# Kernel tuning notes

Hardware: AMD Instinct MI355X
Metric: run time of the kernel (lower is better)

The kernel has to match this reference:

```python
import jax, jax.numpy as jnp
from jax import lax
import numpy as np

C_IN, C_OUT, K, STRIDE, PAD = 64, 64, 3, 1, 1
EPS = 1e-5


def setup_inputs() -> dict:
    key = jax.random.key(0)
    ks = jax.random.split(key, 6)
    B, H, W = 4, 128, 128
    x = jax.random.normal(ks[0], (B, C_IN, H, W), jnp.float32)
    # small offset weights -> realistic sub-pixel offsets
    offset_w = jax.random.normal(ks[1], (2 * K * K, C_IN, K, K), jnp.float32) * 0.01
    offset_b = jax.random.normal(ks[2], (2 * K * K,), jnp.float32) * 0.01
    dcn_w = jax.random.normal(ks[3], (C_OUT, C_IN, K, K), jnp.float32) / np.sqrt(C_IN * K * K)
    gamma = jax.random.uniform(ks[4], (C_OUT,), jnp.float32, 0.5, 1.5)
    beta = jax.random.normal(ks[5], (C_OUT,), jnp.float32) * 0.1
    return dict(x=x, offset_w=offset_w, offset_b=offset_b, dcn_w=dcn_w, gamma=gamma, beta=beta)


def _bilinear_sample(xb, py, px):
    # xb: (C,H,W); py,px: (K2,Ho,Wo) absolute sample coords (may be out of bounds)
    H, W = xb.shape[1], xb.shape[2]
    y0 = jnp.floor(py); x0 = jnp.floor(px)
    wy = py - y0  # frac weights
    wx = px - x0

    def gather(yi, xi):
        yc = jnp.clip(yi, 0, H - 1).astype(jnp.int32)
        xc = jnp.clip(xi, 0, W - 1).astype(jnp.int32)
        v = xb[:, yc, xc]  # (C,K2,Ho,Wo)
        valid = ((yi >= 0) & (yi <= H - 1) & (xi >= 0) & (xi <= W - 1)).astype(xb.dtype)
        return v * valid[None]

    return (gather(y0, x0) * ((1 - wy) * (1 - wx))[None]
            + gather(y0, x0 + 1) * ((1 - wy) * wx)[None]
            + gather(y0 + 1, x0) * (wy * (1 - wx))[None]
            + gather(y0 + 1, x0 + 1) * (wy * wx)[None])  # (C,K2,Ho,Wo)


def reference(x, offset_w, offset_b, dcn_w, gamma, beta):
    B, C, H, W = x.shape
    K2 = K * K
    # offset conv (standard conv, NCHW)
    offset = lax.conv_general_dilated(
        x, offset_w, (STRIDE, STRIDE), [(PAD, PAD), (PAD, PAD)],
        dimension_numbers=("NCHW", "OIHW", "NCHW")) + offset_b[None, :, None, None]
    Ho, Wo = offset.shape[2], offset.shape[3]
    off = offset.reshape(B, K2, 2, Ho, Wo)  # interleaved (dy, dx) per tap
    dy, dx = off[:, :, 0], off[:, :, 1]
    # base sampling grid: out_pos*stride - pad + kernel tap index
    hs = (jnp.arange(Ho) * STRIDE - PAD).astype(x.dtype)
    ws = (jnp.arange(Wo) * STRIDE - PAD).astype(x.dtype)
    ki, kj = jnp.meshgrid(jnp.arange(K), jnp.arange(K), indexing="ij")
    ki = ki.reshape(K2).astype(x.dtype)
    kj = kj.reshape(K2).astype(x.dtype)
    py = dy + hs[None, None, :, None] + ki[None, :, None, None]  # (B,K2,Ho,Wo)
    px = dx + ws[None, None, None, :] + kj[None, :, None, None]

    sampled = jax.vmap(_bilinear_sample)(x, py, px)  # (B,C,K2,Ho,Wo)
    out = jnp.einsum("bckhw,ock->bohw", sampled, dcn_w.reshape(dcn_w.shape[0], C, K2))

    # BatchNorm (training-mode batch stats) + ReLU
    mean = out.mean((0, 2, 3))
    var = out.var((0, 2, 3))
    out = (out - mean[None, :, None, None]) * lax.rsqrt(var + EPS)[None, :, None, None]
    out = out * gamma[None, :, None, None] + beta[None, :, None, None]
    return jnp.maximum(out, 0.0)
```

## Files before the change

### kernel.cpp

```cpp
#include <hip/hip_runtime.h>

#define HW   16384
#define NPX  65536

typedef unsigned short u16;
typedef unsigned int   u32;
typedef short bf16x8 __attribute__((ext_vector_type(8)));
typedef float f32x4  __attribute__((ext_vector_type(4)));

__device__ __forceinline__ u16 f2b(float f) {
    u32 u = __float_as_uint(f);
    return (u16)((u + 0x7FFFu + ((u >> 16) & 1u)) >> 16);
}
__device__ __forceinline__ float blo(u32 u) { return __uint_as_float(u << 16); }
__device__ __forceinline__ float bhi(u32 u) { return __uint_as_float(u & 0xffff0000u); }

__device__ __forceinline__ u32 comb(u32 a00, u32 a01, u32 a10, u32 a11,
                                    float w00, float w01, float w10, float w11) {
    float lo = fmaf(w11, blo(a11), fmaf(w10, blo(a10), fmaf(w01, blo(a01), w00 * blo(a00))));
    float hi = fmaf(w11, bhi(a11), fmaf(w10, bhi(a10), fmaf(w01, bhi(a01), w00 * bhi(a00))));
    return __builtin_amdgcn_perm(__float_as_uint(hi) + 0x8000u,
                                 __float_as_uint(lo) + 0x8000u, 0x07060302u);
}

#define MFMA __builtin_amdgcn_mfma_f32_16x16x32_bf16
#define NTL(p) __builtin_nontemporal_load(p)

__global__ __launch_bounds__(256)
void k_pre(const float* __restrict__ x, const float* __restrict__ dw,
           const float* __restrict__ ow, u16* __restrict__ xh,
           u16* __restrict__ wtd, u16* __restrict__ wto,
           float* __restrict__ sums) {
    int tid = threadIdx.x;
    int bid = blockIdx.x;
    if (bid >= 512) {
        if (bid == 539) {
            for (int i = tid; i < 1024; i += 256) sums[i] = 0.f;
            return;
        }
        int gid = (bid - 512) * 256 + tid;
        if (gid >= 108 * 64) return;
        int fid = gid >> 6, lane = gid & 63;
        int mi = lane & 15, quad = lane >> 4;
        u32 w[4];
        if (fid < 72) {
            int tap = fid >> 3, rem = fid & 7;
            int ks = rem >> 2, nt = rem & 3;
            int n = nt * 16 + mi;
            int cb = ks * 32 + quad * 8;
#pragma unroll
            for (int i = 0; i < 4; ++i) {
                u32 lo = f2b(dw[(n * 64 + cb + 2 * i) * 9 + tap]);
                u32 hi = f2b(dw[(n * 64 + cb + 2 * i + 1) * 9 + tap]);
                w[i] = lo | (hi << 16);
            }
            *((int4*)wtd + (fid << 6) + lane) = make_int4(w[0], w[1], w[2], w[3]);
        } else {
            int f2 = fid - 72;
            int tap = f2 >> 2, rem = f2 & 3;
            int ks = rem >> 1, nt = rem & 1;
            int n = nt * 16 + mi;
            int cb = ks * 32 + quad * 8;
#pragma unroll
            for (int i = 0; i < 4; ++i) {
                u32 lo = (n < 18) ? f2b(ow[(n * 64 + cb + 2 * i) * 9 + tap]) : 0u;
                u32 hi = (n < 18) ? f2b(ow[(n * 64 + cb + 2 * i + 1) * 9 + tap]) : 0u;
                w[i] = lo | (hi << 16);
            }
            *((int4*)wto + (f2 << 6) + lane) = make_int4(w[0], w[1], w[2], w[3]);
        }
        return;
    }
    __shared__ u16 tile[64][138];
    int p0  = bid * 128;
    int b   = p0 >> 14;
    int hw0 = p0 & (HW - 1);
    int pxq = (tid & 31) * 4;
    int rr  = tid >> 5;
    const float* src = x + (size_t)b * 64 * HW + hw0 + pxq;
#pragma unroll
    for (int i = 0; i < 8; ++i) {
        int c = i * 8 + rr;
        float4 v = *(const float4*)(src + (size_t)c * HW);
        ushort4 h;
        h.x = f2b(v.x); h.y = f2b(v.y); h.z = f2b(v.z); h.w = f2b(v.w);
        *(ushort4*)&tile[c][pxq] = h;
    }
    __syncthreads();
    int sub = tid & 3;
#pragma unroll
    for (int j = 0; j < 2; ++j) {
        int px = j * 64 + (tid >> 2);
        u32 w[8];
#pragma unroll
        for (int t = 0; t < 8; ++t) {
            int c = sub * 16 + 2 * t;
            w[t] = (u32)tile[c][px] | ((u32)tile[c + 1][px] << 16);
        }
        u16* dst = xh + (size_t)(p0 + px) * 64 + sub * 16;
        *(int4*)dst       = make_int4(w[0], w[1], w[2], w[3]);
        *(int4*)(dst + 8) = make_int4(w[4], w[5], w[6], w[7]);
    }
}

__global__ __launch_bounds__(256, 6)
void k_main(const u16* __restrict__ xh, const u16* __restrict__ wto,
            const u16* __restrict__ wtd, const float* __restrict__ ob,
            float* __restrict__ out, float* __restrict__ sums) {
    __shared__ float offs[2][18][34];
    __shared__ float so[64][33];

    int tid = threadIdx.x;
    int vb  = (blockIdx.x & 7) * 256 + (blockIdx.x >> 3);
    int p0  = vb * 32;
    int b   = p0 >> 14;
    int hw0 = p0 & (HW - 1);
    int y   = hw0 >> 7;
    int x0  = hw0 & 127;
    int wave = tid >> 6, lane = tid & 63;
    int mi = lane & 15, quad = lane >> 4;
    int ks = wave >> 1;
    int m0 = (wave & 1) << 4;
    int xcol = x0 + m0 + mi;
    int koff = ks * 32 + quad * 8;
    const u16* xb = xh + (size_t)b * HW * 64;
    const bf16x8* WO = (const bf16x8*)wto;
    const bf16x8* WD = (const bf16x8*)wtd;

    f32x4 oa0 = {0.f, 0.f, 0.f, 0.f}, oa1 = {0.f, 0.f, 0.f, 0.f};
#pragma unroll
    for (int tap = 0; tap < 9; ++tap) {
        int yy = y + tap / 3 - 1;
        int xx = xcol + tap % 3 - 1;
        int yc = min(max(yy, 0), 127), xc = min(max(xx, 0), 127);
        bool valid = ((unsigned)yy < 128u) && ((unsigned)xx < 128u);
        int4 a = *(const int4*)(xb + ((yc << 7) + xc) * 64 + koff);
        if (!valid) a = make_int4(0, 0, 0, 0);
        bf16x8 af = __builtin_bit_cast(bf16x8, a);
        oa0 = MFMA(af, NTL(&WO[((tap * 4 + ks * 2 + 0) << 6) + lane]), oa0, 0, 0, 0);
        oa1 = MFMA(af, NTL(&WO[((tap * 4 + ks * 2 + 1) << 6) + lane]), oa1, 0, 0, 0);
    }
    {
        float bias0 = (ks == 0) ? ob[mi] : 0.f;
#pragma unroll
        for (int r = 0; r < 4; ++r)
            offs[ks][mi][m0 + quad * 4 + r] = oa0[r] + bias0;
        if (mi < 2) {
            float bias1 = (ks == 0) ? ob[16 + mi] : 0.f;
#pragma unroll
            for (int r = 0; r < 4; ++r)
                offs[ks][16 + mi][m0 + quad * 4 + r] = oa1[r] + bias1;
        }
    }
    __syncthreads();

    int pxl = m0 + mi;
    float offv[18];
#pragma unroll
    for (int m = 0; m < 18; ++m)
        offv[m] = offs[0][m][pxl] + offs[1][m][pxl];

    float fy = (float)y, fx = (float)xcol;
    f32x4 acc0 = {0.f,0.f,0.f,0.f}, acc1 = {0.f,0.f,0.f,0.f};
    f32x4 acc2 = {0.f,0.f,0.f,0.f}, acc3 = {0.f,0.f,0.f,0.f};

#pragma unroll
    for (int tap = 0; tap < 9; ++tap) {
        float py  = offv[2 * tap]     + fy + (float)(tap / 3 - 1);
        float pf  = offv[2 * tap + 1] + fx + (float)(tap % 3 - 1);
        float y0f = floorf(py), x0f = floorf(pf);
        float wy  = py - y0f,   wx  = pf - x0f;
        int   iy0 = (int)y0f,   ix0 = (int)x0f;
        float vy0 = (y0f >=  0.f && y0f <= 127.f) ? 1.f : 0.f;
        float vy1 = (y0f >= -1.f && y0f <= 126.f) ? 1.f : 0.f;
        float vx0 = (x0f >=  0.f && x0f <= 127.f) ? 1.f : 0.f;
        float vx1 = (x0f >= -1.f && x0f <= 126.f) ? 1.f : 0.f;
        int cy0 = min(max(iy0, 0), 127), cy1 = min(max(iy0 + 1, 0), 127);
        int cx0 = min(max(ix0, 0), 127), cx1 = min(max(ix0 + 1, 0), 127);
        float w00 = (1.f - wy) * (1.f - wx) * vy0 * vx0;
        float w01 = (1.f - wy) * wx * vy0 * vx1;
        float w10 = wy * (1.f - wx) * vy1 * vx0;
        float w11 = wy * wx * vy1 * vx1;
        int4 v00 = *(const int4*)(xb + ((cy0 << 7) + cx0) * 64 + koff);
        int4 v01 = *(const int4*)(xb + ((cy0 << 7) + cx1) * 64 + koff);
        int4 v10 = *(const int4*)(xb + ((cy1 << 7) + cx0) * 64 + koff);
        int4 v11 = *(const int4*)(xb + ((cy1 << 7) + cx1) * 64 + koff);
        int4 r;
        r.x = comb(v00.x, v01.x, v10.x, v11.x, w00, w01, w10, w11);
        r.y = comb(v00.y, v01.y, v10.y, v11.y, w00, w01, w10, w11);
        r.z = comb(v00.z, v01.z, v10.z, v11.z, w00, w01, w10, w11);
        r.w = comb(v00.w, v01.w, v10.w, v11.w, w00, w01, w10, w11);
        bf16x8 a = __builtin_bit_cast(bf16x8, r);
        acc0 = MFMA(a, NTL(&WD[((tap * 8 + ks * 4 + 0) << 6) + lane]), acc0, 0, 0, 0);
        acc1 = MFMA(a, NTL(&WD[((tap * 8 + ks * 4 + 1) << 6) + lane]), acc1, 0, 0, 0);
        acc2 = MFMA(a, NTL(&WD[((tap * 8 + ks * 4 + 2) << 6) + lane]), acc2, 0, 0, 0);
        acc3 = MFMA(a, NTL(&WD[((tap * 8 + ks * 4 + 3) << 6) + lane]), acc3, 0, 0, 0);
    }

    if (ks == 1) {
#pragma unroll
        for (int r = 0; r < 4; ++r) {
            so[ 0 + mi][m0 + quad * 4 + r] = acc0[r];
            so[16 + mi][m0 + quad * 4 + r] = acc1[r];
            so[32 + mi][m0 + quad * 4 + r] = acc2[r];
            so[48 + mi][m0 + quad * 4 + r] = acc3[r];
        }
    }
    __syncthreads();
    if (ks == 0) {
#pragma unroll
        for (int r = 0; r < 4; ++r) {
            so[ 0 + mi][m0 + quad * 4 + r] += acc0[r];
            so[16 + mi][m0 + quad * 4 + r] += acc1[r];
            so[32 + mi][m0 + quad * 4 + r] += acc2[r];
            so[48 + mi][m0 + quad * 4 + r] += acc3[r];
        }
    }
    __syncthreads();

    int n  = tid >> 2;
    int c4 = tid & 3;
    int pl = c4 * 8;
    float s = 0.f, q = 0.f;
    float vals[8];
#pragma unroll
    for (int i = 0; i < 8; ++i) {
        float v = so[n][pl + i];
        vals[i] = v;
        s += v;
        q = fmaf(v, v, q);
    }
    float* dst = out + (size_t)(b * 64 + n) * HW + (y << 7) + x0 + pl;
    *(float4*)dst       = make_float4(vals[0], vals[1], vals[2], vals[3]);
    *(float4*)(dst + 4) = make_float4(vals[4], vals[5], vals[6], vals[7]);

    s += __shfl_xor(s, 1); s += __shfl_xor(s, 2);
    q += __shfl_xor(q, 1); q += __shfl_xor(q, 2);
    if (c4 == 0) {
        float* sb = sums + (blockIdx.x & 7) * 128;
        atomicAdd(&sb[n], s);
        atomicAdd(&sb[64 + n], q);
    }
}

__global__ __launch_bounds__(256)
void k_bn(float* __restrict__ out, const float* __restrict__ sums,
          const float* __restrict__ gamma, const float* __restrict__ beta) {
    int i4 = blockIdx.x * 256 + threadIdx.x;
    int e  = i4 << 2;
    int o  = (e >> 14) & 63;
    float sm = 0.f, sq = 0.f;
#pragma unroll
    for (int s8 = 0; s8 < 8; ++s8) {
        sm += sums[s8 * 128 + o];
        sq += sums[s8 * 128 + 64 + o];
    }
    const float n = 65536.f;
    float mean = sm / n;
    float var  = fmaxf(sq / n - mean * mean, 0.f);
    float sc   = rsqrtf(var + 1e-5f) * gamma[o];
    float sh   = beta[o] - mean * sc;
    float4 v = *(const float4*)&out[e];
    v.x = fmaxf(fmaf(v.x, sc, sh), 0.f);
    v.y = fmaxf(fmaf(v.y, sc, sh), 0.f);
    v.z = fmaxf(fmaf(v.z, sc, sh), 0.f);
    v.w = fmaxf(fmaf(v.w, sc, sh), 0.f);
    *(float4*)&out[e] = v;
}

extern "C" void kernel_launch(void* const* d_in, const int* in_sizes, int n_in,
                              void* d_out, int out_size, void* d_ws, size_t ws_size,
                              hipStream_t stream) {
    const float* x     = (const float*)d_in[0];
    const float* ow    = (const float*)d_in[1];
    const float* ob    = (const float*)d_in[2];
    const float* dw    = (const float*)d_in[3];
    const float* gamma = (const float*)d_in[4];
    const float* beta  = (const float*)d_in[5];
    float* out = (float*)d_out;
    char*  wsb = (char*)d_ws;
    u16*   xh   = (u16*)wsb;
    u16*   wtd  = (u16*)(wsb + 8388608);
    u16*   wto  = (u16*)(wsb + 8462336);
    float* sums = (float*)(wsb + 8499200);

    k_pre<<<540, 256, 0, stream>>>(x, dw, ow, xh, wtd, wto, sums);
    k_main<<<2048, 256, 0, stream>>>(xh, wto, wtd, ob, out, sums);
    k_bn<<<4096, 256, 0, stream>>>(out, sums, gamma, beta);
}
```

Baseline: 144.9 us.

## Stage 5x36 input window in LDS for offset conv and bilinear gathers

```diff
diff --git a/kernel.cpp b/kernel.cpp
--- a/kernel.cpp
+++ b/kernel.cpp
@@ -24,7 +24,6 @@
 }
 
 #define MFMA __builtin_amdgcn_mfma_f32_16x16x32_bf16
-#define NTL(p) __builtin_nontemporal_load(p)
 
 __global__ __launch_bounds__(256)
 void k_pre(const float* __restrict__ x, const float* __restrict__ dw,
@@ -103,10 +102,11 @@
     }
 }
 
-__global__ __launch_bounds__(256, 6)
+__global__ __launch_bounds__(256, 4)
 void k_main(const u16* __restrict__ xh, const u16* __restrict__ wto,
             const u16* __restrict__ wtd, const float* __restrict__ ob,
             float* __restrict__ out, float* __restrict__ sums) {
+    __shared__ __align__(16) char win[25920];
     __shared__ float offs[2][18][34];
     __shared__ float so[64][33];
 
@@ -122,10 +122,27 @@
     int ks = wave >> 1;
     int m0 = (wave & 1) << 4;
     int xcol = x0 + m0 + mi;
-    int koff = ks * 32 + quad * 8;
+    int koffu = ks * 32 + quad * 8;
+    int boff  = ks * 64 + quad * 16;
+    int ywin = y - 2, xwin = x0 - 2;
     const u16* xb = xh + (size_t)b * HW * 64;
     const bf16x8* WO = (const bf16x8*)wto;
     const bf16x8* WD = (const bf16x8*)wtd;
+
+#pragma unroll
+    for (int wr = 0; wr < 5; ++wr) {
+        int r = ywin + wr;
+        if ((unsigned)r < 128u) {
+            for (int u = tid; u < 288; u += 256) {
+                int wc = u >> 3, ch = u & 7;
+                int c = xwin + wc;
+                if ((unsigned)c < 128u)
+                    *(int4*)(win + (wr * 36 + wc) * 144 + ch * 16) =
+                        *(const int4*)(xb + (((r << 7) + c) << 6) + ch * 8);
+            }
+        }
+    }
+    __syncthreads();
 
     f32x4 oa0 = {0.f, 0.f, 0.f, 0.f}, oa1 = {0.f, 0.f, 0.f, 0.f};
 #pragma unroll
@@ -134,11 +151,12 @@
         int xx = xcol + tap % 3 - 1;
         int yc = min(max(yy, 0), 127), xc = min(max(xx, 0), 127);
         bool valid = ((unsigned)yy < 128u) && ((unsigned)xx < 128u);
-        int4 a = *(const int4*)(xb + ((yc << 7) + xc) * 64 + koff);
+        int wr = yc - ywin, wc = xc - xwin;
+        int4 a = *(const int4*)(win + (wr * 36 + wc) * 144 + boff);
         if (!valid) a = make_int4(0, 0, 0, 0);
         bf16x8 af = __builtin_bit_cast(bf16x8, a);
-        oa0 = MFMA(af, NTL(&WO[((tap * 4 + ks * 2 + 0) << 6) + lane]), oa0, 0, 0, 0);
-        oa1 = MFMA(af, NTL(&WO[((tap * 4 + ks * 2 + 1) << 6) + lane]), oa1, 0, 0, 0);
+        oa0 = MFMA(af, WO[((tap * 4 + ks * 2 + 0) << 6) + lane], oa0, 0, 0, 0);
+        oa1 = MFMA(af, WO[((tap * 4 + ks * 2 + 1) << 6) + lane], oa1, 0, 0, 0);
     }
     {
         float bias0 = (ks == 0) ? ob[mi] : 0.f;
@@ -163,6 +181,17 @@
     float fy = (float)y, fx = (float)xcol;
     f32x4 acc0 = {0.f,0.f,0.f,0.f}, acc1 = {0.f,0.f,0.f,0.f};
     f32x4 acc2 = {0.f,0.f,0.f,0.f}, acc3 = {0.f,0.f,0.f,0.f};
+
+    auto rd = [&](int cy, int cx) -> int4 {
+        int wr = cy - ywin, wc = cx - xwin;
+        int4 v;
+        if (((unsigned)wr < 5u) && ((unsigned)wc < 36u)) {
+            v = *(const int4*)(win + (wr * 36 + wc) * 144 + boff);
+        } else {
+            v = *(const int4*)(xb + (((cy << 7) + cx) << 6) + koffu);
+        }
+        return v;
+    };
 
 #pragma unroll
     for (int tap = 0; tap < 9; ++tap) {
@@ -181,20 +210,21 @@
         float w01 = (1.f - wy) * wx * vy0 * vx1;
         float w10 = wy * (1.f - wx) * vy1 * vx0;
         float w11 = wy * wx * vy1 * vx1;
-        int4 v00 = *(const int4*)(xb + ((cy0 << 7) + cx0) * 64 + koff);
-        int4 v01 = *(const int4*)(xb + ((cy0 << 7) + cx1) * 64 + koff);
-        int4 v10 = *(const int4*)(xb + ((cy1 << 7) + cx0) * 64 + koff);
-        int4 v11 = *(const int4*)(xb + ((cy1 << 7) + cx1) * 64 + koff);
+        int4 v00 = rd(cy0, cx0);
+        int4 v01 = rd(cy0, cx1);
+        int4 v10 = rd(cy1, cx0);
+        int4 v11 = rd(cy1, cx1);
         int4 r;
         r.x = comb(v00.x, v01.x, v10.x, v11.x, w00, w01, w10, w11);
         r.y = comb(v00.y, v01.y, v10.y, v11.y, w00, w01, w10, w11);
         r.z = comb(v00.z, v01.z, v10.z, v11.z, w00, w01, w10, w11);
         r.w = comb(v00.w, v01.w, v10.w, v11.w, w00, w01, w10, w11);
         bf16x8 a = __builtin_bit_cast(bf16x8, r);
-        acc0 = MFMA(a, NTL(&WD[((tap * 8 + ks * 4 + 0) << 6) + lane]), acc0, 0, 0, 0);
-        acc1 = MFMA(a, NTL(&WD[((tap * 8 + ks * 4 + 1) << 6) + lane]), acc1, 0, 0, 0);
-        acc2 = MFMA(a, NTL(&WD[((tap * 8 + ks * 4 + 2) << 6) + lane]), acc2, 0, 0, 0);
-        acc3 = MFMA(a, NTL(&WD[((tap * 8 + ks * 4 + 3) << 6) + lane]), acc3, 0, 0, 0);
+        int tb = tap * 8 + ks * 4;
+        acc0 = MFMA(a, WD[((tb + 0) << 6) + lane], acc0, 0, 0, 0);
+        acc1 = MFMA(a, WD[((tb + 1) << 6) + lane], acc1, 0, 0, 0);
+        acc2 = MFMA(a, WD[((tb + 2) << 6) + lane], acc2, 0, 0, 0);
+        acc3 = MFMA(a, WD[((tb + 3) << 6) + lane], acc3, 0, 0, 0);
     }
 
     if (ks == 1) {
```

New measurement: 123.4 us. 1.17x faster.
